# Kernel optimization log

Measured on AMD Instinct MI355X. Metric: run time of the kernel, lower is better.

Reference implementation:

```python
import jax, jax.numpy as jnp
import numpy as np

N = 50000
E = 800000
IN_DIM = 256
HID = 64
HEADS0 = 4
HEADS1 = 1
NUM_CLASSES = 64
NEG_SLOPE = 0.2


def setup_inputs() -> dict:
    key = jax.random.key(0)
    ks = jax.random.split(key, 9)
    x = jax.random.normal(ks[0], (N, IN_DIM), dtype=jnp.float32)
    src0 = jax.random.randint(ks[1], (E,), 0, N, dtype=jnp.int32)
    dst0 = jax.random.randint(ks[2], (E,), 0, N, dtype=jnp.int32)
    src1 = jax.random.randint(ks[3], (E,), 0, N, dtype=jnp.int32)
    dst1 = jax.random.randint(ks[4], (E,), 0, N, dtype=jnp.int32)
    # layer 0: fc (share_weights -> single W), attn vector per head
    W0 = jax.random.normal(ks[5], (IN_DIM, HEADS0 * HID), dtype=jnp.float32) * (1.0 / np.sqrt(IN_DIM))
    attn0 = jax.random.normal(ks[6], (HEADS0, HID), dtype=jnp.float32) * (1.0 / np.sqrt(HID))
    # layer 1 (final): input dim = HID*HEADS0, out = NUM_CLASSES per head
    W1 = jax.random.normal(ks[7], (HID * HEADS0, HEADS1 * NUM_CLASSES), dtype=jnp.float32) * (1.0 / np.sqrt(HID * HEADS0))
    attn1 = jax.random.normal(ks[8], (HEADS1, NUM_CLASSES), dtype=jnp.float32) * (1.0 / np.sqrt(NUM_CLASSES))
    return {"x": x, "W0": W0, "attn0": attn0, "W1": W1, "attn1": attn1,
            "src0": src0, "dst0": dst0, "src1": src1, "dst1": dst1}


def gatv2_conv(h, W, attn, src, dst, n_nodes):
    """DGL GATv2Conv with share_weights=True, bias=False, residual=False.
    h: [N, Fin], W: [Fin, H*D], attn: [H, D]. Returns [N, H, D]."""
    H, D = attn.shape
    feat = (h @ W).reshape(n_nodes, H, D)          # [N, H, D]
    fs = feat[src]                                  # [E, H, D] gather src
    fd = feat[dst]                                  # [E, H, D] gather dst
    # e_ij = a^T LeakyReLU(W h_i + W h_j)
    e = jnp.einsum('ehd,hd->eh', jax.nn.leaky_relu(fs + fd, NEG_SLOPE), attn)  # [E, H]
    # edge softmax over incoming edges of each dst node (stable)
    m = jax.ops.segment_max(e, dst, num_segments=n_nodes)    # [N, H]
    ex = jnp.exp(e - m[dst])                                  # [E, H]
    s = jax.ops.segment_sum(ex, dst, num_segments=n_nodes)   # [N, H]
    alpha = ex / s[dst]                                       # [E, H]
    out = jax.ops.segment_sum(alpha[:, :, None] * fs, dst, num_segments=n_nodes)  # [N, H, D]
    return out


def reference(x, W0, attn0, W1, attn1, src0, dst0, src1, dst1):
    h = gatv2_conv(x, W0, attn0, src0, dst0, N)      # [N, 4, 64]
    h = jax.nn.elu(h)                                 # layer activation
    h = h.reshape(N, HEADS0 * HID)                    # flatten(1)
    h = gatv2_conv(h, W1, attn1, src1, dst1, N)       # [N, 1, 64], no activation
    logits = h.mean(axis=1)                           # mean over heads -> [N, 64]
    return logits
```

## Files before the change

### kernel.cpp

```cpp
#include <hip/hip_runtime.h>

#define N_NODES 50000
#define E_EDGES 800000
#define NEG_SLOPE 0.2f
#define NSL 8
#define SLN (NSL * N_NODES)
#define ROWS_PAD 50048
#define GB0 782
#define EB 3125
#define NBE0 12500
#define CAP 16
#define WIB 40

typedef __attribute__((ext_vector_type(8))) _Float16 f16x8;
typedef __attribute__((ext_vector_type(4))) float f32x4;
typedef __attribute__((ext_vector_type(4))) _Float16 half4v;
typedef __attribute__((ext_vector_type(2))) _Float16 half2v;

union H4 { half4v h4; half2v h2[2]; unsigned u[2]; };

__device__ __forceinline__ void gload_lds16(const void* g, void* l) {
    __builtin_amdgcn_global_load_lds((__attribute__((address_space(1))) void*)g,
                                     (__attribute__((address_space(3))) void*)l, 16, 0, 0);
}

#define LOG2E 1.4426950408889634f

__device__ __forceinline__ float score4(half4v g, half4v fd, const H4& A6, const H4& A4) {
    H4 Z; Z.h4 = g + fd;
    H4 B; B.u[0] = Z.u[0] & 0x7FFF7FFFu; B.u[1] = Z.u[1] & 0x7FFF7FFFu;
    float p = __builtin_amdgcn_fdot2(Z.h2[0], A6.h2[0], 0.0f, false);
    p = __builtin_amdgcn_fdot2(Z.h2[1], A6.h2[1], p, false);
    p = __builtin_amdgcn_fdot2(B.h2[0], A4.h2[0], p, false);
    p = __builtin_amdgcn_fdot2(B.h2[1], A4.h2[1], p, false);
    return p;
}

__device__ __forceinline__ void wimg_one(const float* W, _Float16* img, int Nc, int i) {
    int col = i >> 5, chunk = i & 31;
    int CT = Nc >> 4;
    int kb = chunk >> 2, ct = col >> 4;
    int li = (col & 15) + (chunk & 3) * 16;
    size_t base = ((size_t)kb * CT + ct) * 512 + li * 8;
    half4v v0, v1;
#pragma unroll
    for (int e = 0; e < 4; ++e) v0[e] = (_Float16)W[(size_t)(chunk * 8 + e) * Nc + col];
#pragma unroll
    for (int e = 0; e < 4; ++e) v1[e] = (_Float16)W[(size_t)(chunk * 8 + 4 + e) * Nc + col];
    *(half4v*)&img[base]     = v0;
    *(half4v*)&img[base + 4] = v1;
}


__global__ void k_scat_wimg(const int* __restrict__ src0, const int* __restrict__ dst0,
                            const int* __restrict__ src1, const int* __restrict__ dst1,
                            int* __restrict__ cnt_s, unsigned short* __restrict__ buck,
                            const float* __restrict__ W0, const float* __restrict__ W1,
                            _Float16* __restrict__ img0, _Float16* __restrict__ img1) {
    if (blockIdx.x < 2 * EB) {
        int layer = (blockIdx.x >= EB) ? 1 : 0;
        int bi = blockIdx.x - layer * EB;
        int slice = bi & (NSL - 1);
        int i = bi * 256 + threadIdx.x;
        int s, d;
        if (layer == 0) {
            s = __builtin_nontemporal_load(&src0[i]);
            d = __builtin_nontemporal_load(&dst0[i]);
        } else {
            s = __builtin_nontemporal_load(&src1[i]);
            d = __builtin_nontemporal_load(&dst1[i]);
        }
        size_t sn = (size_t)layer * SLN + slice * N_NODES + d;
        int pos = atomicAdd(&cnt_s[sn], 1);
        if (pos < CAP) buck[(sn << 4) + pos] = (unsigned short)s;
        return;
    }
    int gtid = (blockIdx.x - 2 * EB) * 256 + threadIdx.x;
    if (gtid < 256 * 32) wimg_one(W0, img0, 256, gtid);
    else if (gtid < 256 * 32 + 64 * 32) wimg_one(W1, img1, 64, gtid - 256 * 32);
}


__global__ __launch_bounds__(256, 4) void mfma_gemm0(const float* __restrict__ X,
                                                     const _Float16* __restrict__ Bimg,
                                                     _Float16* __restrict__ C, int M) {
    constexpr int CT = 16;
    __shared__ __align__(16) _Float16 AsF[4 * 512];
    __shared__ __align__(16) _Float16 Bs[CT * 512];

    const int t = threadIdx.x;
    const int w = t >> 6;
    const int lane = t & 63;
    const int r16 = lane & 15;
    const int kg = lane >> 4;
    const int bm = blockIdx.x * 64;
    const int arow = bm + w * 16 + r16;
    const bool rv = (arow < M);
    const float* xsrc = X + (size_t)arow * 256 + kg * 8;

    f32x4 acc[CT];
#pragma unroll
    for (int j = 0; j < CT; ++j) acc[j] = (f32x4){0.f, 0.f, 0.f, 0.f};

    for (int kb = 0; kb < 8; ++kb) {
        float4 v0 = make_float4(0.f, 0.f, 0.f, 0.f);
        float4 v1 = make_float4(0.f, 0.f, 0.f, 0.f);
        if (rv) {
            v0 = *(const float4*)(xsrc + kb * 32);
            v1 = *(const float4*)(xsrc + kb * 32 + 4);
        }
        f16x8 af;
        af[0] = (_Float16)v0.x; af[1] = (_Float16)v0.y;
        af[2] = (_Float16)v0.z; af[3] = (_Float16)v0.w;
        af[4] = (_Float16)v1.x; af[5] = (_Float16)v1.y;
        af[6] = (_Float16)v1.z; af[7] = (_Float16)v1.w;
        *(f16x8*)&AsF[t * 8] = af;
#pragma unroll
        for (int p = 0; p < CT / 4; ++p)
            gload_lds16(Bimg + kb * CT * 512 + p * 2048 + t * 8, &Bs[p * 2048 + w * 512]);
        __syncthreads();

        const f16x8 aF = *(const f16x8*)&AsF[t * 8];
#pragma unroll
        for (int ct = 0; ct < CT; ++ct) {
            const f16x8 b = *(const f16x8*)&Bs[ct * 512 + lane * 8];
            acc[ct] = __builtin_amdgcn_mfma_f32_16x16x32_f16(aF, b, acc[ct], 0, 0, 0);
        }
        __syncthreads();
    }

#pragma unroll
    for (int r = 0; r < 4; ++r) {
        int row = bm + w * 16 + kg * 4 + r;
        if (row < M) {
#pragma unroll
            for (int ct = 0; ct < CT; ++ct)
                C[(size_t)row * 256 + ct * 16 + r16] = (_Float16)acc[ct][r];
        }
    }
}


__device__ __forceinline__ int bucket_prefix(const int* __restrict__ cnt_s,
                                             int base, int node, int lane, int& excl) {
    int c = 0;
    if (lane < NSL) {
        c = cnt_s[base + lane * N_NODES + node];
        c = (c > CAP) ? CAP : c;
    }
    excl = 0;
    int total = 0;
#pragma unroll
    for (int ss = 0; ss < NSL; ++ss) {
        int v = __shfl(c, ss);
        if (ss < (lane & 7)) excl += v;
        total += v;
    }
    return total;
}

__device__ __forceinline__ int bucket_offset(const unsigned short* __restrict__ buck,
                                             int base, int node, int excl, int rr,
                                             int total, int sh) {
    int sl = 0;
#pragma unroll
    for (int ss = 1; ss < NSL; ++ss) {
        int e = __shfl(excl, ss);
        if (rr >= e) sl = ss;
    }
    int eS = __shfl(excl, sl);
    int v = 0;
    if (rr < total)
        v = buck[(((size_t)base + sl * N_NODES + node) << 4) + (rr - eS)];
    return v << sh;
}


__global__ __launch_bounds__(256) void gat_edge0(const _Float16* __restrict__ feat,
                                                 const float* __restrict__ attn,
                                                 const int* __restrict__ cnt_s,
                                                 const unsigned short* __restrict__ buck,
                                                 _Float16* __restrict__ h0img) {
    const int lane = threadIdx.x & 63;
    const int node = blockIdx.x * 4 + (threadIdx.x >> 6);
    if (node >= N_NODES) return;
    const int dbase = ((lane >> 4) << 6) + (lane & 15) * 4;
    const float4 a = *(const float4*)&attn[dbase];
    H4 A6, A4;
    A6.h4 = (half4v){(_Float16)(0.6f * LOG2E * a.x), (_Float16)(0.6f * LOG2E * a.y),
                     (_Float16)(0.6f * LOG2E * a.z), (_Float16)(0.6f * LOG2E * a.w)};
    A4.h4 = (half4v){(_Float16)(0.4f * LOG2E * a.x), (_Float16)(0.4f * LOG2E * a.y),
                     (_Float16)(0.4f * LOG2E * a.z), (_Float16)(0.4f * LOG2E * a.w)};
    const char* fbase = (const char*)feat + dbase * 2;
    const half4v fd4 = *(const half4v*)(fbase + ((size_t)node << 9));

    int excl;
    const int total = bucket_prefix(cnt_s, 0, node, lane, excl);

    float s = 0.f, ax = 0.f, ay = 0.f, az = 0.f, aw = 0.f;
    for (int b = 0; b < total; b += 64) {
        const int my_ofs = bucket_offset(buck, 0, node, excl, b + lane, total, 9);
        const int ch = min(total - b, 64);
        int i = 0;
        for (; i + 7 < ch; i += 8) {
            half4v g[8];
            float p[8];
#pragma unroll
            for (int k = 0; k < 8; ++k) g[k] = *(const half4v*)(fbase + __shfl(my_ofs, i + k));
#pragma unroll
            for (int k = 0; k < 8; ++k) p[k] = score4(g[k], fd4, A6, A4);
#pragma unroll
            for (int r = 1; r <= 8; r <<= 1)
#pragma unroll
                for (int k = 0; k < 8; ++k) p[k] += __shfl_xor(p[k], r);
            float e[8];
#pragma unroll
            for (int k = 0; k < 8; ++k) e[k] = __builtin_amdgcn_exp2f(p[k]);
#pragma unroll
            for (int k = 0; k < 8; ++k) {
                s  += e[k];
                ax += e[k] * (float)g[k][0];
                ay += e[k] * (float)g[k][1];
                az += e[k] * (float)g[k][2];
                aw += e[k] * (float)g[k][3];
            }
        }
        if (i + 3 < ch) {
            half4v g[4];
            float p[4];
#pragma unroll
            for (int k = 0; k < 4; ++k) g[k] = *(const half4v*)(fbase + __shfl(my_ofs, i + k));
#pragma unroll
            for (int k = 0; k < 4; ++k) p[k] = score4(g[k], fd4, A6, A4);
#pragma unroll
            for (int r = 1; r <= 8; r <<= 1)
#pragma unroll
                for (int k = 0; k < 4; ++k) p[k] += __shfl_xor(p[k], r);
#pragma unroll
            for (int k = 0; k < 4; ++k) {
                float e = __builtin_amdgcn_exp2f(p[k]);
                s  += e;
                ax += e * (float)g[k][0];
                ay += e * (float)g[k][1];
                az += e * (float)g[k][2];
                aw += e * (float)g[k][3];
            }
            i += 4;
        }
        for (; i < ch; ++i) {
            half4v g0 = *(const half4v*)(fbase + __shfl(my_ofs, i));
            float p0 = score4(g0, fd4, A6, A4);
            p0 += __shfl_xor(p0, 1);
            p0 += __shfl_xor(p0, 2);
            p0 += __shfl_xor(p0, 4);
            p0 += __shfl_xor(p0, 8);
            float e0 = __builtin_amdgcn_exp2f(p0);
            s  += e0;
            ax += e0 * (float)g0[0];
            ay += e0 * (float)g0[1];
            az += e0 * (float)g0[2];
            aw += e0 * (float)g0[3];
        }
    }
    float inv = (total > 0) ? (1.0f / s) : 0.f;
    half4v o;
    float v;
    v = ax * inv; o[0] = (_Float16)((v > 0.f) ? v : (__expf(v) - 1.f));
    v = ay * inv; o[1] = (_Float16)((v > 0.f) ? v : (__expf(v) - 1.f));
    v = az * inv; o[2] = (_Float16)((v > 0.f) ? v : (__expf(v) - 1.f));
    v = aw * inv; o[3] = (_Float16)((v > 0.f) ? v : (__expf(v) - 1.f));
    const int rtg = node >> 4;
    const int kb = dbase >> 5;
    const int li = (node & 15) + ((dbase >> 3) & 3) * 16;
    const size_t idx = ((size_t)rtg * 8 + kb) * 512 + li * 8 + (dbase & 7);
    *(half4v*)&h0img[idx] = o;
}


__global__ __launch_bounds__(256, 4) void mfma_gemm1(const _Float16* __restrict__ Aimg,
                                                     const _Float16* __restrict__ Bimg,
                                                     _Float16* __restrict__ C, int M) {
    constexpr int CT = 4;
    __shared__ __align__(16) _Float16 AsF[4 * 512];
    __shared__ __align__(16) _Float16 Bs[CT * 512];

    const int t = threadIdx.x;
    const int w = t >> 6;
    const int lane = t & 63;
    const int r16 = lane & 15;
    const int kg = lane >> 4;
    const int bm = blockIdx.x * 64;

    f32x4 acc[CT];
#pragma unroll
    for (int j = 0; j < CT; ++j) acc[j] = (f32x4){0.f, 0.f, 0.f, 0.f};

    const size_t abase = ((size_t)(blockIdx.x * 4 + w)) * 8 * 512;

    for (int kb = 0; kb < 8; ++kb) {
        gload_lds16(Aimg + abase + kb * 512 + lane * 8, &AsF[w * 512]);
        gload_lds16(Bimg + kb * CT * 512 + t * 8, &Bs[w * 512]);
        __syncthreads();

        const f16x8 aF = *(const f16x8*)&AsF[w * 512 + lane * 8];
#pragma unroll
        for (int ct = 0; ct < CT; ++ct) {
            const f16x8 b = *(const f16x8*)&Bs[ct * 512 + lane * 8];
            acc[ct] = __builtin_amdgcn_mfma_f32_16x16x32_f16(aF, b, acc[ct], 0, 0, 0);
        }
        __syncthreads();
    }

#pragma unroll
    for (int r = 0; r < 4; ++r) {
        int row = bm + w * 16 + kg * 4 + r;
        if (row < M) {
#pragma unroll
            for (int ct = 0; ct < CT; ++ct)
                C[(size_t)row * 64 + ct * 16 + r16] = (_Float16)acc[ct][r];
        }
    }
}


__global__ __launch_bounds__(256) void gat_edge1(const _Float16* __restrict__ feat,
                                                 const float* __restrict__ attn,
                                                 const int* __restrict__ cnt_s,
                                                 const unsigned short* __restrict__ buck,
                                                 float* __restrict__ out) {
    const int lane = threadIdx.x & 63;
    const int node = blockIdx.x * 4 + (threadIdx.x >> 6);
    if (node >= N_NODES) return;
    const int g = lane >> 4;
    const int d0 = (lane & 15) * 4;
    const float4 a = *(const float4*)&attn[d0];
    H4 A6, A4;
    A6.h4 = (half4v){(_Float16)(0.6f * LOG2E * a.x), (_Float16)(0.6f * LOG2E * a.y),
                     (_Float16)(0.6f * LOG2E * a.z), (_Float16)(0.6f * LOG2E * a.w)};
    A4.h4 = (half4v){(_Float16)(0.4f * LOG2E * a.x), (_Float16)(0.4f * LOG2E * a.y),
                     (_Float16)(0.4f * LOG2E * a.z), (_Float16)(0.4f * LOG2E * a.w)};
    const char* fbase = (const char*)feat + d0 * 2;
    const half4v fd4 = *(const half4v*)(fbase + ((size_t)node << 7));

    int excl;
    const int total = bucket_prefix(cnt_s, SLN, node, lane, excl);

    float s = 0.f, ax = 0.f, ay = 0.f, az = 0.f, aw = 0.f;
    for (int b = 0; b < total; b += 64) {
        const int my_ofs = bucket_offset(buck, SLN, node, excl, b + lane, total, 7);
        const int ch = min(total - b, 64);
        const int rounds = (ch + 3) >> 2;
        for (int m = 0; m < rounds; m += 2) {
            const int e0 = 4 * m + g;
            const int e1 = e0 + 4;
            const int o0 = __shfl(my_ofs, e0 & 63);
            const int o1 = __shfl(my_ofs, e1 & 63);
            const bool v0 = (e0 < ch);
            const bool v1 = (e1 < ch);
            half4v g0 = *(const half4v*)(fbase + o0);
            half4v g1 = *(const half4v*)(fbase + o1);
            float p0 = score4(g0, fd4, A6, A4);
            float p1 = score4(g1, fd4, A6, A4);
            p0 += __shfl_xor(p0, 1); p1 += __shfl_xor(p1, 1);
            p0 += __shfl_xor(p0, 2); p1 += __shfl_xor(p1, 2);
            p0 += __shfl_xor(p0, 4); p1 += __shfl_xor(p1, 4);
            p0 += __shfl_xor(p0, 8); p1 += __shfl_xor(p1, 8);
            float e0f = v0 ? __builtin_amdgcn_exp2f(p0) : 0.f;
            float e1f = v1 ? __builtin_amdgcn_exp2f(p1) : 0.f;
            s  += e0f + e1f;
            ax += e0f * (float)g0[0] + e1f * (float)g1[0];
            ay += e0f * (float)g0[1] + e1f * (float)g1[1];
            az += e0f * (float)g0[2] + e1f * (float)g1[2];
            aw += e0f * (float)g0[3] + e1f * (float)g1[3];
        }
    }
#pragma unroll
    for (int off = 16; off <= 32; off <<= 1) {
        s  += __shfl_xor(s, off);
        ax += __shfl_xor(ax, off);
        ay += __shfl_xor(ay, off);
        az += __shfl_xor(az, off);
        aw += __shfl_xor(aw, off);
    }
    if (g == 0) {
        float inv = (total > 0) ? (1.0f / s) : 0.f;
        float4 o = make_float4(ax * inv, ay * inv, az * inv, aw * inv);
        *(float4*)&out[(size_t)node * 64 + d0] = o;
    }
}


extern "C" void kernel_launch(void* const* d_in, const int* in_sizes, int n_in,
                              void* d_out, int out_size, void* d_ws, size_t ws_size,
                              hipStream_t stream) {
    const float* x     = (const float*)d_in[0];
    const float* W0    = (const float*)d_in[1];
    const float* attn0 = (const float*)d_in[2];
    const float* W1    = (const float*)d_in[3];
    const float* attn1 = (const float*)d_in[4];
    const int*   src0  = (const int*)d_in[5];
    const int*   dst0  = (const int*)d_in[6];
    const int*   src1  = (const int*)d_in[7];
    const int*   dst1  = (const int*)d_in[8];
    float* out = (float*)d_out;

    _Float16* h0img  = (_Float16*)d_ws;
    _Float16* feat0h = h0img + (size_t)ROWS_PAD * 256;
    _Float16* W0img  = feat0h + (size_t)N_NODES * 256;
    _Float16* W1img  = W0img + 256 * 256;
    _Float16* feat1h = feat0h;

    int* cnt_s = (int*)(W1img + 64 * 256);
    unsigned short* buck = (unsigned short*)(cnt_s + 2 * SLN);

    hipMemsetAsync(cnt_s, 0, 2 * SLN * sizeof(int), stream);

    k_scat_wimg<<<2 * EB + WIB, 256, 0, stream>>>(src0, dst0, src1, dst1, cnt_s, buck,
                                                  W0, W1, W0img, W1img);

    mfma_gemm0<<<GB0, 256, 0, stream>>>(x, W0img, feat0h, N_NODES);

    gat_edge0<<<NBE0, 256, 0, stream>>>(feat0h, attn0, cnt_s, buck, h0img);

    mfma_gemm1<<<GB0, 256, 0, stream>>>(h0img, W1img, feat1h, N_NODES);

    gat_edge1<<<NBE0, 256, 0, stream>>>(feat1h, attn1, cnt_s, buck, out);
}
```

Measured before the change: 225.0 us.

## Fuse edge bucketing into GEMM0 launch and inline bucket counts

Edge scatter/bucketing blocks now run in the same launch as the layer-0 GEMM, and the small W-image conversion moves to its own tiny kernel. Per-bucket counters are stored inline in the first 4 bytes of each 32-byte bucket, so the count and indices share a cache line and the separate counter array goes away. CAP drops from 16 to 14 to make room for the counter. This aims to overlap atomic-heavy scatter work with the compute-bound GEMM and cut one memory stream in the edge kernels. The cost is a larger memset and a lower overflow capacity per slice, which could drop edges for high in-degree nodes.

New measurement: 258.0 us. 1.15x slower.

```diff
diff --git a/kernel.cpp b/kernel.cpp
--- a/kernel.cpp
+++ b/kernel.cpp
@@ -9,7 +9,7 @@
 #define GB0 782
 #define EB 3125
 #define NBE0 12500
-#define CAP 16
+#define CAP 14
 #define WIB 40
 
 typedef __attribute__((ext_vector_type(8))) _Float16 f16x8;
@@ -52,14 +52,30 @@
 }
 
 
-__global__ void k_scat_wimg(const int* __restrict__ src0, const int* __restrict__ dst0,
-                            const int* __restrict__ src1, const int* __restrict__ dst1,
-                            int* __restrict__ cnt_s, unsigned short* __restrict__ buck,
-                            const float* __restrict__ W0, const float* __restrict__ W1,
-                            _Float16* __restrict__ img0, _Float16* __restrict__ img1) {
-    if (blockIdx.x < 2 * EB) {
-        int layer = (blockIdx.x >= EB) ? 1 : 0;
-        int bi = blockIdx.x - layer * EB;
+__global__ void k_wimg(const float* __restrict__ W0, const float* __restrict__ W1,
+                       _Float16* __restrict__ img0, _Float16* __restrict__ img1) {
+    int gtid = blockIdx.x * 256 + threadIdx.x;
+    if (gtid < 256 * 32) wimg_one(W0, img0, 256, gtid);
+    else if (gtid < 256 * 32 + 64 * 32) wimg_one(W1, img1, 64, gtid - 256 * 32);
+}
+
+
+__global__ __launch_bounds__(256, 4) void k_gemm0_scat(const float* __restrict__ X,
+                                                       const _Float16* __restrict__ Bimg,
+                                                       _Float16* __restrict__ C, int M,
+                                                       const int* __restrict__ src0,
+                                                       const int* __restrict__ dst0,
+                                                       const int* __restrict__ src1,
+                                                       const int* __restrict__ dst1,
+                                                       unsigned short* __restrict__ buck) {
+    constexpr int CT = 16;
+    __shared__ __align__(16) _Float16 AsF[4 * 512];
+    __shared__ __align__(16) _Float16 Bs[CT * 512];
+
+    if (blockIdx.x >= GB0) {
+        int hb = blockIdx.x - GB0;
+        int layer = (hb >= EB) ? 1 : 0;
+        int bi = hb - layer * EB;
         int slice = bi & (NSL - 1);
         int i = bi * 256 + threadIdx.x;
         int s, d;
@@ -71,22 +87,10 @@
             d = __builtin_nontemporal_load(&dst1[i]);
         }
         size_t sn = (size_t)layer * SLN + slice * N_NODES + d;
-        int pos = atomicAdd(&cnt_s[sn], 1);
-        if (pos < CAP) buck[(sn << 4) + pos] = (unsigned short)s;
+        int pos = atomicAdd((int*)(buck + (sn << 4)), 1);
+        if (pos < CAP) buck[(sn << 4) + 2 + pos] = (unsigned short)s;
         return;
     }
-    int gtid = (blockIdx.x - 2 * EB) * 256 + threadIdx.x;
-    if (gtid < 256 * 32) wimg_one(W0, img0, 256, gtid);
-    else if (gtid < 256 * 32 + 64 * 32) wimg_one(W1, img1, 64, gtid - 256 * 32);
-}
-
-
-__global__ __launch_bounds__(256, 4) void mfma_gemm0(const float* __restrict__ X,
-                                                     const _Float16* __restrict__ Bimg,
-                                                     _Float16* __restrict__ C, int M) {
-    constexpr int CT = 16;
-    __shared__ __align__(16) _Float16 AsF[4 * 512];
-    __shared__ __align__(16) _Float16 Bs[CT * 512];
 
     const int t = threadIdx.x;
     const int w = t >> 6;
@@ -141,11 +145,11 @@
 }
 
 
-__device__ __forceinline__ int bucket_prefix(const int* __restrict__ cnt_s,
+__device__ __forceinline__ int bucket_prefix(const unsigned short* __restrict__ buck,
                                              int base, int node, int lane, int& excl) {
     int c = 0;
     if (lane < NSL) {
-        c = cnt_s[base + lane * N_NODES + node];
+        c = *(const int*)(buck + (((size_t)base + lane * N_NODES + node) << 4));
         c = (c > CAP) ? CAP : c;
     }
     excl = 0;
@@ -171,14 +175,13 @@
     int eS = __shfl(excl, sl);
     int v = 0;
     if (rr < total)
-        v = buck[(((size_t)base + sl * N_NODES + node) << 4) + (rr - eS)];
+        v = buck[(((size_t)base + sl * N_NODES + node) << 4) + 2 + (rr - eS)];
     return v << sh;
 }
 
 
 __global__ __launch_bounds__(256) void gat_edge0(const _Float16* __restrict__ feat,
                                                  const float* __restrict__ attn,
-                                                 const int* __restrict__ cnt_s,
                                                  const unsigned short* __restrict__ buck,
                                                  _Float16* __restrict__ h0img) {
     const int lane = threadIdx.x & 63;
@@ -195,7 +198,7 @@
     const half4v fd4 = *(const half4v*)(fbase + ((size_t)node << 9));
 
     int excl;
-    const int total = bucket_prefix(cnt_s, 0, node, lane, excl);
+    const int total = bucket_prefix(buck, 0, node, lane, excl);
 
     float s = 0.f, ax = 0.f, ay = 0.f, az = 0.f, aw = 0.f;
     for (int b = 0; b < total; b += 64) {
@@ -325,7 +328,6 @@
 
 __global__ __launch_bounds__(256) void gat_edge1(const _Float16* __restrict__ feat,
                                                  const float* __restrict__ attn,
-                                                 const int* __restrict__ cnt_s,
                                                  const unsigned short* __restrict__ buck,
                                                  float* __restrict__ out) {
     const int lane = threadIdx.x & 63;
@@ -343,7 +345,7 @@
     const half4v fd4 = *(const half4v*)(fbase + ((size_t)node << 7));
 
     int excl;
-    const int total = bucket_prefix(cnt_s, SLN, node, lane, excl);
+    const int total = bucket_prefix(buck, SLN, node, lane, excl);
 
     float s = 0.f, ax = 0.f, ay = 0.f, az = 0.f, aw = 0.f;
     for (int b = 0; b < total; b += 64) {
@@ -410,19 +412,18 @@
     _Float16* W1img  = W0img + 256 * 256;
     _Float16* feat1h = feat0h;
 
-    int* cnt_s = (int*)(W1img + 64 * 256);
-    unsigned short* buck = (unsigned short*)(cnt_s + 2 * SLN);
-
-    hipMemsetAsync(cnt_s, 0, 2 * SLN * sizeof(int), stream);
-
-    k_scat_wimg<<<2 * EB + WIB, 256, 0, stream>>>(src0, dst0, src1, dst1, cnt_s, buck,
-                                                  W0, W1, W0img, W1img);
-
-    mfma_gemm0<<<GB0, 256, 0, stream>>>(x, W0img, feat0h, N_NODES);
-
-    gat_edge0<<<NBE0, 256, 0, stream>>>(feat0h, attn0, cnt_s, buck, h0img);
+    unsigned short* buck = (unsigned short*)(W1img + 64 * 256);
+
+    hipMemsetAsync(buck, 0, (size_t)2 * SLN * 32, stream);
+
+    k_wimg<<<WIB, 256, 0, stream>>>(W0, W1, W0img, W1img);
+
+    k_gemm0_scat<<<GB0 + 2 * EB, 256, 0, stream>>>(x, W0img, feat0h, N_NODES,
+                                                   src0, dst0, src1, dst1, buck);
+
+    gat_edge0<<<NBE0, 256, 0, stream>>>(feat0h, attn0, buck, h0img);
 
     mfma_gemm1<<<GB0, 256, 0, stream>>>(h0img, W1img, feat1h, N_NODES);
 
-    gat_edge1<<<NBE0, 256, 0, stream>>>(feat1h, attn1, cnt_s, buck, out);
-}
+    gat_edge1<<<NBE0, 256, 0, stream>>>(feat1h, attn1, buck, out);
+}
```
